# Optimization experiments

Measured on AMD Instinct MI355X. Metric: run time of the kernel, lower is better.

The kernel has to match this reference:

```python
import jax, jax.numpy as jnp
import numpy as np

VOCAB = 50000
E = 256      # text_embed_dim
K = 512      # num_kernels
KS = 9       # kernel_size
L = 8192     # num labels
B, T = 8, 2048
PAD = KS // 2


def setup_inputs() -> dict:
    key = jax.random.key(0)
    ks = jax.random.split(key, 9)
    ids = jax.random.randint(ks[0], (B, T), 0, VOCAB)
    mask = jnp.ones((B, T), dtype=jnp.int32)  # unused by forward, kept for signature parity
    target = (jax.random.uniform(ks[1], (B, L)) < 0.01).astype(jnp.float32)
    embed_w = jax.random.normal(ks[2], (VOCAB, E), jnp.float32) * 0.02
    conv_w = jax.random.normal(ks[3], (K, E, KS), jnp.float32) * (1.0 / np.sqrt(E * KS))
    conv_b = jnp.zeros((K,), jnp.float32)
    U_w = jax.random.normal(ks[4], (L, K), jnp.float32) * (1.0 / np.sqrt(K))
    final_w = jax.random.normal(ks[5], (L, K), jnp.float32) * (1.0 / np.sqrt(K))
    final_b = jnp.zeros((L,), jnp.float32)
    return {"ids": ids, "mask": mask, "G": 0, "target": target,
            "embed_w": embed_w, "conv_w": conv_w, "conv_b": conv_b,
            "U_w": U_w, "final_w": final_w, "final_b": final_b}


def _forward(ids, embed_w, conv_w, conv_b, U_w, final_w, final_b):
    # embed + (dropout=identity in eval) -> [B, E, T]
    x = embed_w[ids].transpose(0, 2, 1)
    # same-padded Conv1d, then ReLU -> text_feats [B, T, K]
    y = jax.lax.conv_general_dilated(x, conv_w, (1,), [(PAD, PAD)],
                                     dimension_numbers=("NCH", "OIH", "NCH"))
    feats = jax.nn.relu(y + conv_b[None, :, None]).transpose(0, 2, 1)
    # label-wise attention: alpha = softmax(U.weight @ feats^T, dim=2) -> [B, L, T]
    scores = jnp.einsum("lk,btk->blt", U_w, feats)
    alpha = jax.nn.softmax(scores, axis=2)
    # attended features per label -> [B, L, K]
    attn = jnp.einsum("blt,btk->blk", alpha, feats)
    # label-wise dot with final.weight + bias -> logits [B, L]
    yhat = jnp.einsum("blk,lk->bl", attn, final_w) + final_b
    return yhat


def _bce_with_logits(yhat, target):
    # mean over all elements, numerically stable
    return jnp.mean(jnp.maximum(yhat, 0) - yhat * target + jnp.log1p(jnp.exp(-jnp.abs(yhat))))


def reference(ids, mask, G, target, embed_w, conv_w, conv_b, U_w, final_w, final_b):
    yhat = _forward(ids, embed_w, conv_w, conv_b, U_w, final_w, final_b)
    loss = _bce_with_logits(yhat, target)
    return yhat, loss
```

## Files before the change

### kernel.cpp

```cpp
#include <hip/hip_runtime.h>
#include <hip/hip_bf16.h>
#include <cstdint>

#define B_ 8
#define T_ 2048
#define E_ 256
#define K_ 512
#define KS_ 9
#define L_ 8192
#define PAD_ 4
#define TP_ (T_ + 2 * PAD_)
#define KK_ (E_ * KS_)

#define FEAT_SCALE 64.0f
#define W_SCALE 16.0f
#define INV_SS 9.765625e-4f
#define INV_SS_LOG2E 1.40888719e-3f

typedef __bf16 bf16x8 __attribute__((ext_vector_type(8)));
typedef float f32x4 __attribute__((ext_vector_type(4)));
typedef float f32x16 __attribute__((ext_vector_type(16)));
typedef int i32x4 __attribute__((ext_vector_type(4)));
typedef int i32x8 __attribute__((ext_vector_type(8)));

__device__ __forceinline__ unsigned short f2bf(float f) {
  union { float f; unsigned int u; } a; a.f = f;
  unsigned int r = (a.u + 0x7FFFu + ((a.u >> 16) & 1u)) >> 16;
  return (unsigned short)r;
}

__device__ __forceinline__ unsigned char f2fp8(float v) {
  return (unsigned char)(__builtin_amdgcn_cvt_pk_fp8_f32(v, v, 0, false) & 0xFF);
}

__device__ __forceinline__ unsigned int pk4_fp8(float a, float b, float c, float d) {
  int v = __builtin_amdgcn_cvt_pk_fp8_f32(a, b, 0, false);
  v = __builtin_amdgcn_cvt_pk_fp8_f32(c, d, v, true);
  return (unsigned int)v;
}

__device__ __forceinline__ void gld_lds16(const void* g, void* l) {
  __builtin_amdgcn_global_load_lds(
      (const __attribute__((address_space(1))) unsigned int*)g,
      (__attribute__((address_space(3))) unsigned int*)l, 16, 0, 0);
}

__device__ __forceinline__ f32x4 mfma_bf16(bf16x8 a, bf16x8 b, f32x4 c) {
  return __builtin_amdgcn_mfma_f32_16x16x32_bf16(a, b, c, 0, 0, 0);
}

__device__ __forceinline__ f32x16 mfma_sc64(i32x8 a, i32x8 b, f32x16 c) {
  return __builtin_amdgcn_mfma_scale_f32_32x32x64_f8f6f4(a, b, c, 0, 0, 0, 127, 0, 127);
}

__device__ __forceinline__ int f_off(int t, int k) {
  return ((t >> 6) * 32768) + (((k >> 4) * 64 + (t & 63)) << 4) + (k & 15);
}
__device__ __forceinline__ int w_off(int l, int k) {
  return ((l >> 7) * 65536) + (((k >> 4) * 128 + (l & 127)) << 4) + (k & 15);
}

__global__ __launch_bounds__(256) void k_embed(const int* __restrict__ ids,
                                               const float* __restrict__ emb,
                                               unsigned short* __restrict__ xpad) {
  int gid = blockIdx.x * 256 + threadIdx.x;
  int row = gid >> 6;
  int e4 = (gid & 63) << 2;
  int b = row / TP_;
  int tp = row - b * TP_;
  float4 v = make_float4(0.f, 0.f, 0.f, 0.f);
  if (tp >= PAD_ && tp < T_ + PAD_) {
    int id = ids[b * T_ + tp - PAD_];
    v = *(const float4*)(emb + (size_t)id * E_ + e4);
  }
  ushort4 o;
  o.x = f2bf(v.x); o.y = f2bf(v.y); o.z = f2bf(v.z); o.w = f2bf(v.w);
  *(ushort4*)(xpad + (size_t)row * E_ + e4) = o;
}

__global__ __launch_bounds__(256) void k_wt(const float* __restrict__ conv_w,
                                            unsigned short* __restrict__ wt) {
  int kk = blockIdx.x * 256 + threadIdx.x;
  int k = blockIdx.y;
  int j = kk >> 8, e = kk & 255;
  wt[(size_t)k * KK_ + kk] = f2bf(conv_w[(k * E_ + e) * KS_ + j]);
}

__global__ __launch_bounds__(256) void k_cast(const float* __restrict__ U_w,
                                              const float* __restrict__ F_w,
                                              unsigned char* __restrict__ u8,
                                              unsigned char* __restrict__ f8) {
  int gid = blockIdx.x * 256 + threadIdx.x;
  const float* src = blockIdx.y ? F_w : U_w;
  unsigned char* dst = blockIdx.y ? f8 : u8;
  int l = gid >> 6;
  int k0 = (gid & 63) << 3;
  const float* s = src + (size_t)l * K_ + k0;
  float4 v0 = *(const float4*)(s);
  float4 v1 = *(const float4*)(s + 4);
  uint2 o;
  o.x = pk4_fp8(v0.x * W_SCALE, v0.y * W_SCALE, v0.z * W_SCALE, v0.w * W_SCALE);
  o.y = pk4_fp8(v1.x * W_SCALE, v1.y * W_SCALE, v1.z * W_SCALE, v1.w * W_SCALE);
  *(uint2*)(dst + w_off(l, k0)) = o;
}

__global__ __launch_bounds__(512, 4) void k_conv(const unsigned short* __restrict__ xpad,
                                                 const unsigned short* __restrict__ wt,
                                                 const float* __restrict__ conv_b,
                                                 unsigned char* __restrict__ feats) {
  __shared__ char At[2][16384];
  __shared__ char Bt[2][16384];
  const int tid = threadIdx.x;
  const int lane = tid & 63;
  const int q = lane >> 4, c = lane & 15;
  const int w = tid >> 6;
  const int wi = w >> 1, wj = w & 1;
  const int b = blockIdx.z;
  const int t0 = blockIdx.y * 128;
  const int n0 = blockIdx.x * 128;

  const char* xb = (const char*)(xpad + (size_t)b * TP_ * E_);
  const char* wb = (const char*)wt;

  const char* asrc[2]; const char* bsrc[2]; int ldso[2];
#pragma unroll
  for (int rnd = 0; rnd < 2; ++rnd) {
    int u = rnd * 512 + tid;
    int r = u >> 3;
    int j = (u & 7) ^ (r & 7);
    asrc[rnd] = xb + (size_t)(t0 + r) * 512 + j * 16;
    bsrc[rnd] = wb + (size_t)(n0 + r) * (KK_ * 2) + j * 16;
    ldso[rnd] = u * 16;
  }

  int offA[2][2], offB[4][2];
#pragma unroll
  for (int li = 0; li < 2; ++li) {
    int r = wi * 32 + li * 16 + c;
#pragma unroll
    for (int h = 0; h < 2; ++h) offA[li][h] = r * 128 + (((4 * h + q) ^ (r & 7)) << 4);
  }
#pragma unroll
  for (int ti = 0; ti < 4; ++ti) {
    int r = wj * 64 + ti * 16 + c;
#pragma unroll
    for (int h = 0; h < 2; ++h) offB[ti][h] = r * 128 + (((4 * h + q) ^ (r & 7)) << 4);
  }

  f32x4 acc[2][4];
  f32x4 zero = {0.f, 0.f, 0.f, 0.f};
#pragma unroll
  for (int i = 0; i < 2; ++i)
#pragma unroll
    for (int j = 0; j < 4; ++j) acc[i][j] = zero;

#pragma unroll
  for (int rnd = 0; rnd < 2; ++rnd) {
    gld_lds16(asrc[rnd], At[0] + ldso[rnd]);
    gld_lds16(bsrc[rnd], Bt[0] + ldso[rnd]);
  }

  for (int it = 0; it < 36; ++it) {
    const int bsel = it & 1;
    __syncthreads();
    if (it != 35) {
      const int kkc = (it + 1) * 64;
      const int aofs = (kkc >> 8) * 512 + (kkc & 255) * 2;
      const int bofs = kkc * 2;
#pragma unroll
      for (int rnd = 0; rnd < 2; ++rnd) {
        gld_lds16(asrc[rnd] + aofs, At[bsel ^ 1] + ldso[rnd]);
        gld_lds16(bsrc[rnd] + bofs, Bt[bsel ^ 1] + ldso[rnd]);
      }
    }
    const char* aB = At[bsel];
    const char* bB = Bt[bsel];
#pragma unroll
    for (int h = 0; h < 2; ++h) {
      bf16x8 afr[2], bfr[4];
#pragma unroll
      for (int li = 0; li < 2; ++li) afr[li] = *(const bf16x8*)(aB + offA[li][h]);
#pragma unroll
      for (int ti = 0; ti < 4; ++ti) bfr[ti] = *(const bf16x8*)(bB + offB[ti][h]);
#pragma unroll
      for (int ti = 0; ti < 4; ++ti)
#pragma unroll
        for (int li = 0; li < 2; ++li)
          acc[li][ti] = mfma_bf16(afr[li], bfr[ti], acc[li][ti]);
    }
  }

  const size_t fbase = (size_t)b * T_ * K_;
#pragma unroll
  for (int ti = 0; ti < 4; ++ti) {
    int k = n0 + wj * 64 + ti * 16 + c;
    float bias = conv_b[k];
#pragma unroll
    for (int li = 0; li < 2; ++li) {
      int tb = t0 + wi * 32 + li * 16 + q * 4;
#pragma unroll
      for (int rr = 0; rr < 4; ++rr) {
        float v = fmaxf(acc[li][ti][rr] + bias, 0.f) * FEAT_SCALE;
        int t = tb + rr;
        feats[fbase + f_off(t, k)] = f2fp8(v);
      }
    }
  }
}

__global__ __launch_bounds__(512, 2) void k_attn(const unsigned char* __restrict__ feats,
                                                 const unsigned char* __restrict__ u8,
                                                 const unsigned char* __restrict__ f8,
                                                 const float* __restrict__ final_b,
                                                 float* __restrict__ out) {
  __shared__ __align__(16) char smem[131072];
  __shared__ float red[512];
  const int tid = threadIdx.x;
  const int lane = tid & 63;
  const int q2 = lane >> 5, c32 = lane & 31;
  const int w = tid >> 6;
  const int wi = w >> 1;
  const int wj = w & 1;
  const int b = blockIdx.y;
  const int l0 = blockIdx.x * 128;

  const unsigned char* fb = feats + (size_t)b * T_ * K_;

  char* Us = smem;
  char* Ws = smem + 65536;
#pragma unroll
  for (int rr = 0; rr < 8; ++rr) {
    gld_lds16(u8 + (size_t)l0 * K_ + rr * 8192 + tid * 16, Us + rr * 8192 + tid * 16);
    gld_lds16(f8 + (size_t)l0 * K_ + rr * 8192 + tid * 16, Ws + rr * 8192 + tid * 16);
  }
  __syncthreads();

  const int arow = wi * 32 + c32;
  const int abase = q2 * 4096 + arow * 16;
  i32x8 uf[8], wf[8];
#pragma unroll
  for (int s = 0; s < 8; ++s) {
    int o0 = abase + s * 8192;
    i32x4 ul = *(const i32x4*)(Us + o0);
    i32x4 uh = *(const i32x4*)(Us + o0 + 2048);
    i32x4 wl = *(const i32x4*)(Ws + o0);
    i32x4 wh = *(const i32x4*)(Ws + o0 + 2048);
    uf[s] = __builtin_shufflevector(ul, uh, 0, 1, 2, 3, 4, 5, 6, 7);
    wf[s] = __builtin_shufflevector(wl, wh, 0, 1, 2, 3, 4, 5, 6, 7);
  }
  __syncthreads();

  char* const Fs0 = smem;
  char* const Fs1 = smem + 32768;
  const unsigned char* fsrc = fb + tid * 16;
#pragma unroll
  for (int rr = 0; rr < 4; ++rr)
    gld_lds16(fsrc + rr * 8192, Fs0 + tid * 16 + rr * 8192);

  const int brow = wj * 32 + c32;
  const int bbase = q2 * 2048 + brow * 16;

  f32x16 accS, accV;
  float num[16], den[16];
#pragma unroll
  for (int r = 0; r < 16; ++r) { accS[r] = 0.f; accV[r] = 0.f; num[r] = 0.f; den[r] = 0.f; }

  for (int tc = 0; tc < 32; ++tc) {
    const int bsel = tc & 1;
    char* const cur = bsel ? Fs1 : Fs0;
    char* const nxt = bsel ? Fs0 : Fs1;
    __syncthreads();
    if (tc != 31) {
      const unsigned char* nsrc = fsrc + (tc + 1) * 32768;
#pragma unroll
      for (int rr = 0; rr < 4; ++rr)
        gld_lds16(nsrc + rr * 8192, nxt + tid * 16 + rr * 8192);
    }
#pragma unroll
    for (int s = 0; s < 8; ++s) {
      i32x4 flo = *(const i32x4*)(cur + bbase + s * 4096);
      i32x4 fhi = *(const i32x4*)(cur + bbase + s * 4096 + 1024);
      i32x8 fa = __builtin_shufflevector(flo, fhi, 0, 1, 2, 3, 4, 5, 6, 7);
      accS = mfma_sc64(uf[s], fa, accS);
      accV = mfma_sc64(wf[s], fa, accV);
    }
#pragma unroll
    for (int r = 0; r < 16; ++r) {
      float p = __builtin_exp2f(accS[r] * INV_SS_LOG2E);
      den[r] += p;
      num[r] += p * accV[r];
      accS[r] = 0.f;
      accV[r] = 0.f;
    }
  }

#pragma unroll
  for (int r = 0; r < 16; ++r) {
#pragma unroll
    for (int m = 1; m < 32; m <<= 1) {
      num[r] += __shfl_xor(num[r], m, 64);
      den[r] += __shfl_xor(den[r], m, 64);
    }
  }
  if (c32 == 0) {
#pragma unroll
    for (int r = 0; r < 16; ++r) {
      int ll = wi * 32 + (r & 3) + 8 * (r >> 2) + 4 * q2;
      red[wj * 256 + ll] = num[r];
      red[wj * 256 + 128 + ll] = den[r];
    }
  }
  __syncthreads();
  if (tid < 128) {
    int l = l0 + tid;
    float n = red[tid] + red[256 + tid];
    float d = red[128 + tid] + red[384 + tid];
    out[(size_t)b * L_ + l] = (n * INV_SS) / d + final_b[l];
  }
}

__global__ __launch_bounds__(256) void k_loss(const float* __restrict__ yhat,
                                              const float* __restrict__ target,
                                              float* __restrict__ loss) {
  int gid = blockIdx.x * 256 + threadIdx.x;
  float s = 0.f;
  for (int i = gid; i < B_ * L_; i += 64 * 256) {
    float y = yhat[i], t = target[i];
    s += fmaxf(y, 0.f) - y * t + log1pf(__expf(-fabsf(y)));
  }
#pragma unroll
  for (int m = 1; m < 64; m <<= 1) s += __shfl_xor(s, m, 64);
  if ((threadIdx.x & 63) == 0) atomicAdd(loss, s * (1.0f / (B_ * L_)));
}

extern "C" void kernel_launch(void* const* d_in, const int* in_sizes, int n_in,
                              void* d_out, int out_size, void* d_ws, size_t ws_size,
                              hipStream_t stream) {
  const int* ids = (const int*)d_in[0];
  const float* target = (const float*)d_in[3];
  const float* emb = (const float*)d_in[4];
  const float* conv_w = (const float*)d_in[5];
  const float* conv_b = (const float*)d_in[6];
  const float* U_w = (const float*)d_in[7];
  const float* F_w = (const float*)d_in[8];
  const float* final_b = (const float*)d_in[9];
  float* out = (float*)d_out;

  char* ws = (char*)d_ws;
  unsigned short* xpad = (unsigned short*)ws;
  size_t off = (size_t)B_ * TP_ * E_ * 2;
  unsigned short* wt = (unsigned short*)(ws + off);
  off += (size_t)K_ * KK_ * 2;
  unsigned char* u8 = (unsigned char*)(ws + off);
  off += (size_t)L_ * K_;
  unsigned char* f8 = (unsigned char*)(ws + off);
  off += (size_t)L_ * K_;
  unsigned char* feats = (unsigned char*)(ws + off);
  off += (size_t)B_ * T_ * K_;
  if (ws_size < off) return;

  k_embed<<<dim3((B_ * TP_ * 64) / 256), 256, 0, stream>>>(ids, emb, xpad);
  k_wt<<<dim3(KK_ / 256, K_), 256, 0, stream>>>(conv_w, wt);
  k_cast<<<dim3((L_ * K_ / 8) / 256, 2), 256, 0, stream>>>(U_w, F_w, u8, f8);
  k_conv<<<dim3(K_ / 128, T_ / 128, B_), 512, 0, stream>>>(xpad, wt, conv_b, feats);
  k_attn<<<dim3(L_ / 128, B_), 512, 0, stream>>>(feats, u8, f8, final_b, out);
  hipMemsetAsync(out + B_ * L_, 0, sizeof(float), stream);
  k_loss<<<dim3(64), 256, 0, stream>>>(out, target, out + B_ * L_);
}
```

Before: 295.6 us.

## Use 32-byte fp8 K-chunk layout and overlap softmax exp with next chunk's MFMAs

Changes the feature and weight fp8 layouts from 16-byte to 32-byte K-groups, so each MFMA operand comes from a single 32-byte LDS read instead of two 16-byte reads plus a shuffle. The attention loop is software-pipelined with two pairs of accumulators: the exp/accumulate for the previous chunk is interleaved with the MFMAs of the current chunk, hiding transcendental latency behind matrix work. This adds register pressure from the doubled accumulators, which matters under launch_bounds(512,2), and the new layout could change LDS bank-conflict patterns.

```diff
diff --git a/kernel.cpp b/kernel.cpp
--- a/kernel.cpp
+++ b/kernel.cpp
@@ -54,10 +54,10 @@
 }
 
 __device__ __forceinline__ int f_off(int t, int k) {
-  return ((t >> 6) * 32768) + (((k >> 4) * 64 + (t & 63)) << 4) + (k & 15);
+  return ((t >> 6) * 32768) + ((k >> 5) * 2048) + ((t & 63) * 32) + (k & 31);
 }
 __device__ __forceinline__ int w_off(int l, int k) {
-  return ((l >> 7) * 65536) + (((k >> 4) * 128 + (l & 127)) << 4) + (k & 15);
+  return ((l >> 7) * 65536) + ((k >> 5) * 4096) + ((l & 127) * 32) + (k & 31);
 }
 
 __global__ __launch_bounds__(256) void k_embed(const int* __restrict__ ids,
@@ -213,7 +213,7 @@
                                                  const unsigned char* __restrict__ f8,
                                                  const float* __restrict__ final_b,
                                                  float* __restrict__ out) {
-  __shared__ __align__(16) char smem[131072];
+  __shared__ __align__(64) char smem[131072];
   __shared__ float red[512];
   const int tid = threadIdx.x;
   const int lane = tid & 63;
@@ -236,17 +236,12 @@
   __syncthreads();
 
   const int arow = wi * 32 + c32;
-  const int abase = q2 * 4096 + arow * 16;
   i32x8 uf[8], wf[8];
 #pragma unroll
   for (int s = 0; s < 8; ++s) {
-    int o0 = abase + s * 8192;
-    i32x4 ul = *(const i32x4*)(Us + o0);
-    i32x4 uh = *(const i32x4*)(Us + o0 + 2048);
-    i32x4 wl = *(const i32x4*)(Ws + o0);
-    i32x4 wh = *(const i32x4*)(Ws + o0 + 2048);
-    uf[s] = __builtin_shufflevector(ul, uh, 0, 1, 2, 3, 4, 5, 6, 7);
-    wf[s] = __builtin_shufflevector(wl, wh, 0, 1, 2, 3, 4, 5, 6, 7);
+    int off = (s * 2 + q2) * 4096 + arow * 32;
+    uf[s] = *(const i32x8*)(Us + off);
+    wf[s] = *(const i32x8*)(Ws + off);
   }
   __syncthreads();
 
@@ -258,41 +253,65 @@
     gld_lds16(fsrc + rr * 8192, Fs0 + tid * 16 + rr * 8192);
 
   const int brow = wj * 32 + c32;
-  const int bbase = q2 * 2048 + brow * 16;
-
-  f32x16 accS, accV;
+  const int bbase = q2 * 2048 + brow * 32;
+
+  f32x16 sA, vA, sB, vB;
   float num[16], den[16];
 #pragma unroll
-  for (int r = 0; r < 16; ++r) { accS[r] = 0.f; accV[r] = 0.f; num[r] = 0.f; den[r] = 0.f; }
-
-  for (int tc = 0; tc < 32; ++tc) {
-    const int bsel = tc & 1;
-    char* const cur = bsel ? Fs1 : Fs0;
-    char* const nxt = bsel ? Fs0 : Fs1;
+  for (int r = 0; r < 16; ++r) { num[r] = 0.f; den[r] = 0.f; }
+
+#define SM1(PS, PV, rr_)                                         \
+  {                                                              \
+    float p_ = __builtin_exp2f(PS[rr_] * INV_SS_LOG2E);          \
+    den[rr_] += p_;                                              \
+    num[rr_] += p_ * PV[rr_];                                    \
+  }
+
+#define CHUNK_BODY(BUF, CS, CV, PS, PV, DO_SM)                   \
+  {                                                              \
+    _Pragma("unroll")                                            \
+    for (int r = 0; r < 16; ++r) { CS[r] = 0.f; CV[r] = 0.f; }   \
+    _Pragma("unroll")                                            \
+    for (int s = 0; s < 8; ++s) {                                \
+      i32x8 fa = *(const i32x8*)(BUF + bbase + s * 4096);        \
+      CS = mfma_sc64(uf[s], fa, CS);                             \
+      CV = mfma_sc64(wf[s], fa, CV);                             \
+      if (DO_SM) { SM1(PS, PV, 2 * s) SM1(PS, PV, 2 * s + 1) }   \
+    }                                                            \
+  }
+
+  __syncthreads();
+#pragma unroll
+  for (int rr = 0; rr < 4; ++rr)
+    gld_lds16(fsrc + 32768 + rr * 8192, Fs1 + tid * 16 + rr * 8192);
+  CHUNK_BODY(Fs0, sA, vA, sB, vB, false)
+
+  for (int tc = 1; tc < 31; tc += 2) {
     __syncthreads();
-    if (tc != 31) {
+    {
       const unsigned char* nsrc = fsrc + (tc + 1) * 32768;
 #pragma unroll
       for (int rr = 0; rr < 4; ++rr)
-        gld_lds16(nsrc + rr * 8192, nxt + tid * 16 + rr * 8192);
-    }
-#pragma unroll
-    for (int s = 0; s < 8; ++s) {
-      i32x4 flo = *(const i32x4*)(cur + bbase + s * 4096);
-      i32x4 fhi = *(const i32x4*)(cur + bbase + s * 4096 + 1024);
-      i32x8 fa = __builtin_shufflevector(flo, fhi, 0, 1, 2, 3, 4, 5, 6, 7);
-      accS = mfma_sc64(uf[s], fa, accS);
-      accV = mfma_sc64(wf[s], fa, accV);
-    }
-#pragma unroll
-    for (int r = 0; r < 16; ++r) {
-      float p = __builtin_exp2f(accS[r] * INV_SS_LOG2E);
-      den[r] += p;
-      num[r] += p * accV[r];
-      accS[r] = 0.f;
-      accV[r] = 0.f;
-    }
-  }
+        gld_lds16(nsrc + rr * 8192, Fs0 + tid * 16 + rr * 8192);
+    }
+    CHUNK_BODY(Fs1, sB, vB, sA, vA, true)
+    __syncthreads();
+    {
+      const unsigned char* nsrc = fsrc + (tc + 2) * 32768;
+#pragma unroll
+      for (int rr = 0; rr < 4; ++rr)
+        gld_lds16(nsrc + rr * 8192, Fs1 + tid * 16 + rr * 8192);
+    }
+    CHUNK_BODY(Fs0, sA, vA, sB, vB, true)
+  }
+
+  __syncthreads();
+  CHUNK_BODY(Fs1, sB, vB, sA, vA, true)
+#pragma unroll
+  for (int r = 0; r < 16; ++r) SM1(sB, vB, r)
+
+#undef CHUNK_BODY
+#undef SM1
 
 #pragma unroll
   for (int r = 0; r < 16; ++r) {
```

After: 513.8 us. 73.8% more time.
